# Optimization experiments

Measured on AMD Instinct MI355X. Metric: run time of the kernel, lower is better.

The kernel has to match this reference:

```python
import jax, jax.numpy as jnp
import numpy as np

B, L, D_MODEL, H = 2, 2048, 1024, 16
HD = D_MODEL // H  # head dim = 64


def setup_inputs() -> dict:
    key = jax.random.key(0)
    ks = jax.random.split(key, 11)
    s = 1.0 / np.sqrt(D_MODEL)
    inp = {
        "Q": jax.random.normal(ks[0], (B, L, D_MODEL), jnp.float32),
        "K": jax.random.normal(ks[1], (B, L, D_MODEL), jnp.float32),
        "V": jax.random.normal(ks[2], (B, L, D_MODEL), jnp.float32),
        "Wq": jax.random.normal(ks[3], (D_MODEL, D_MODEL), jnp.float32) * s,
        "bq": jnp.zeros((D_MODEL,), jnp.float32),
        "Wk": jax.random.normal(ks[4], (D_MODEL, D_MODEL), jnp.float32) * s,
        "bk": jnp.zeros((D_MODEL,), jnp.float32),
        "Wv": jax.random.normal(ks[5], (D_MODEL, D_MODEL), jnp.float32) * s,
        "bv": jnp.zeros((D_MODEL,), jnp.float32),
        "Wo": jax.random.normal(ks[6], (D_MODEL, D_MODEL), jnp.float32) * s,
        "bo": jnp.zeros((D_MODEL,), jnp.float32),
    }
    return inp


def _split_heads(x):
    # [B, L, H*D] -> [B, H, L, D]
    return x.reshape(B, L, H, HD).transpose(0, 2, 1, 3)


def reference(Q, K, V, Wq, bq, Wk, bk, Wv, bv, Wo, bo):
    q = _split_heads(Q @ Wq.T + bq)
    k = _split_heads(K @ Wk.T + bk)
    v = _split_heads(V @ Wv.T + bv)
    scale = 1.0 / jnp.sqrt(jnp.asarray(HD, q.dtype))
    # full [B, H, L, L] score matrix, as in the original bmm->softmax->bmm
    scores = jnp.einsum("bhqd,bhkd->bhqk", q, k) * scale
    attn = jax.nn.softmax(scores, axis=-1)
    o = jnp.einsum("bhqk,bhkd->bhqd", attn, v)
    o = o.transpose(0, 2, 1, 3).reshape(B, L, D_MODEL)  # concat heads
    return o @ Wo.T + bo
```

## Files before the change

### kernel.cpp

```cpp
#include <hip/hip_runtime.h>
#include <math.h>
#include <stdint.h>

typedef __bf16 bf16_t;
typedef __attribute__((ext_vector_type(2))) __bf16 bf16x2;
typedef __attribute__((ext_vector_type(8))) __bf16 bf16x8;
typedef __attribute__((ext_vector_type(4))) float f32x4;
typedef __attribute__((ext_vector_type(16))) float f32x16;
typedef __attribute__((address_space(1))) unsigned int gu32;
typedef __attribute__((address_space(3))) unsigned int lu32;

#define MFMA16(a, b, c) __builtin_amdgcn_mfma_f32_16x16x32_bf16((a), (b), (c), 0, 0, 0)
#define MFMA32(a, b, c) __builtin_amdgcn_mfma_f32_32x32x16_bf16((a), (b), (c), 0, 0, 0)

__device__ __forceinline__ void gll16(const void* g, void* l) {
    __builtin_amdgcn_global_load_lds((const gu32*)(uintptr_t)g,
                                     (lu32*)(uintptr_t)l, 16, 0, 0);
}

__device__ __forceinline__ bf16x8 ld_frag68(const bf16_t* p) {
    union { bf16x8 v; uint2 u[2]; } r;
    r.u[0] = *(const uint2*)p;
    r.u[1] = *(const uint2*)(p + 4);
    return r.v;
}

__global__ __launch_bounds__(256) void convert_all(
    const float* __restrict__ Q, const float* __restrict__ K, const float* __restrict__ V,
    const float* __restrict__ Wq, const float* __restrict__ Wk, const float* __restrict__ Wv,
    const float* __restrict__ Wo, bf16_t* __restrict__ dst) {
    size_t e0 = (size_t)blockIdx.x * 2048;
    const float* src; size_t off;
    if (e0 < 4194304)       { src = Q;  off = e0; }
    else if (e0 < 8388608)  { src = K;  off = e0 - 4194304; }
    else if (e0 < 12582912) { src = V;  off = e0 - 8388608; }
    else if (e0 < 13631488) { src = Wq; off = e0 - 12582912; }
    else if (e0 < 14680064) { src = Wk; off = e0 - 13631488; }
    else if (e0 < 15728640) { src = Wv; off = e0 - 14680064; }
    else                    { src = Wo; off = e0 - 15728640; }
#pragma unroll
    for (int p = 0; p < 2; ++p) {
        int t = p * 1024 + threadIdx.x * 4;
        float4 v = *(const float4*)(src + off + t);
        union { ushort4 u; bf16_t h[4]; } pk;
        pk.h[0] = (bf16_t)v.x; pk.h[1] = (bf16_t)v.y;
        pk.h[2] = (bf16_t)v.z; pk.h[3] = (bf16_t)v.w;
        *(ushort4*)(dst + e0 + t) = pk.u;
    }
}

__global__ __launch_bounds__(256) void qkv_gemm(
    const bf16_t* __restrict__ Qb, const bf16_t* __restrict__ Kb, const bf16_t* __restrict__ Vb,
    const bf16_t* __restrict__ Wqb, const bf16_t* __restrict__ Wkb, const bf16_t* __restrict__ Wvb,
    const float* __restrict__ bq, const float* __restrict__ bk, const float* __restrict__ bv,
    bf16_t* __restrict__ qo, bf16_t* __restrict__ ko, bf16_t* __restrict__ vT) {
    constexpr int Kdim = 1024, N = 1024;
    __shared__ __attribute__((aligned(16))) bf16_t smem[4 * 128 * 64];

    const int tid = threadIdx.x, wave = tid >> 6, lane = tid & 63;
    const int z = blockIdx.z;
    const bf16_t* A = (z == 0) ? Qb : (z == 1) ? Kb : Vb;
    const bf16_t* W = (z == 0) ? Wqb : (z == 1) ? Wkb : Wvb;
    const float* bias = (z == 0) ? bq : (z == 1) ? bk : bv;
    const int bm = blockIdx.x * 128, bn = blockIdx.y * 128;
    const int l16 = lane & 15, quad = lane >> 4;
    const int wm = (wave >> 1) * 64, wn = (wave & 1) * 64;
    const int grow = lane >> 3;
    const int gcol = (((lane & 7) ^ grow)) * 8;
    const int rsw = l16 & 7;

    f32x4 acc[4][4] = {};

    auto stage = [&](int k0, bf16_t* As, bf16_t* Bs) {
#pragma unroll
        for (int j = 0; j < 4; ++j) {
            int chunk = wave * 4 + j;
            int row = chunk * 8 + grow;
            gll16(A + (size_t)(bm + row) * Kdim + k0 + gcol, As + chunk * 512);
            gll16(W + (size_t)(bn + row) * Kdim + k0 + gcol, Bs + chunk * 512);
        }
    };
    auto compute = [&](const bf16_t* As, const bf16_t* Bs) {
#pragma unroll
        for (int ks = 0; ks < 64; ks += 32) {
            const int sl = ((ks >> 3) + quad);
            const int so = (sl ^ rsw) * 8;
            bf16x8 af[4], bf[4];
#pragma unroll
            for (int i = 0; i < 4; ++i)
                af[i] = *(const bf16x8*)&As[(wm + i * 16 + l16) * 64 + so];
#pragma unroll
            for (int i = 0; i < 4; ++i)
                bf[i] = *(const bf16x8*)&Bs[(wn + i * 16 + l16) * 64 + so];
#pragma unroll
            for (int i = 0; i < 4; ++i)
#pragma unroll
                for (int j = 0; j < 4; ++j)
                    acc[i][j] = MFMA16(af[i], bf[j], acc[i][j]);
        }
    };

    stage(0, smem, smem + 8192);
    asm volatile("s_waitcnt vmcnt(0)" ::: "memory");
    __builtin_amdgcn_s_barrier();
    int cur = 0;
    for (int t = 0; t < 15; ++t) {
        bf16_t* nb = smem + (cur ^ 1) * 16384;
        stage((t + 1) * 64, nb, nb + 8192);
        bf16_t* cb = smem + cur * 16384;
        compute(cb, cb + 8192);
        asm volatile("s_waitcnt vmcnt(0)" ::: "memory");
        __builtin_amdgcn_s_barrier();
        cur ^= 1;
    }
    {
        bf16_t* cb = smem + cur * 16384;
        compute(cb, cb + 8192);
    }

    if (z < 2) {
        bf16_t* outp = (z == 0) ? qo : ko;
        const float sc = (z == 0) ? 0.18033688011112042f : 1.0f;
        constexpr int RST = 132;
#pragma unroll
        for (int p = 0; p < 2; ++p) {
            __syncthreads();
            if ((wave >> 1) == p) {
#pragma unroll
                for (int mi = 0; mi < 4; ++mi)
#pragma unroll
                    for (int nj = 0; nj < 4; ++nj) {
                        int col = wn + nj * 16 + l16;
                        float bv_ = bias[bn + col];
#pragma unroll
                        for (int r = 0; r < 4; ++r) {
                            int rp = mi * 16 + quad * 4 + r;
                            smem[rp * RST + col] = (bf16_t)((acc[mi][nj][r] + bv_) * sc);
                        }
                    }
            }
            __syncthreads();
            int rp = tid >> 2;
            int cb2 = (tid & 3) * 32;
            int row = bm + p * 64 + rp;
#pragma unroll
            for (int j = 0; j < 4; ++j) {
                uint2 lo = *(const uint2*)&smem[rp * RST + cb2 + j * 8];
                uint2 hi = *(const uint2*)&smem[rp * RST + cb2 + j * 8 + 4];
                *(uint4*)&outp[(size_t)row * N + bn + cb2 + j * 8] =
                    make_uint4(lo.x, lo.y, hi.x, hi.y);
            }
        }
    } else {
#pragma unroll
        for (int mi = 0; mi < 4; ++mi)
#pragma unroll
            for (int nj = 0; nj < 4; ++nj) {
                int col = bn + wn + nj * 16 + l16;
                int h = col >> 6, d = col & 63;
                float bv_ = bias[col];
                int row0 = bm + wm + mi * 16 + quad * 4;
                int bb = row0 >> 11, l = row0 & 2047;
                int lb = (l & ~12) | ((l & 4) << 1) | ((l & 8) >> 1);
                union { ushort4 u; bf16_t h4[4]; } pk;
#pragma unroll
                for (int r = 0; r < 4; ++r) pk.h4[r] = (bf16_t)(acc[mi][nj][r] + bv_);
                *(ushort4*)&vT[(((size_t)bb * 16 + h) * 64 + d) * 2048 + lb] = pk.u;
            }
    }
}

__global__ __launch_bounds__(256) void out_gemm(const bf16_t* __restrict__ A,
                                                const bf16_t* __restrict__ W,
                                                const float* __restrict__ bias,
                                                float* __restrict__ out) {
    constexpr int Kdim = 1024, N = 1024;
    __shared__ __attribute__((aligned(16))) bf16_t smem[2 * 12288];
    const int tid = threadIdx.x, wave = tid >> 6, lane = tid & 63;
    const int bm = blockIdx.x * 64, bn = blockIdx.y * 128;
    const int l16 = lane & 15, quad = lane >> 4;
    const int wm = (wave >> 1) * 32, wn = (wave & 1) * 64;
    const int grow = lane >> 3;
    const int gcol = (((lane & 7) ^ grow)) * 8;
    const int rsw = l16 & 7;
    f32x4 acc[2][4] = {};

    auto stage = [&](int k0, bf16_t* As, bf16_t* Bs) {
#pragma unroll
        for (int j = 0; j < 2; ++j) {
            int chunk = wave * 2 + j;
            int row = chunk * 8 + grow;
            gll16(A + (size_t)(bm + row) * Kdim + k0 + gcol, As + chunk * 512);
        }
#pragma unroll
        for (int j = 0; j < 4; ++j) {
            int chunk = wave * 4 + j;
            int row = chunk * 8 + grow;
            gll16(W + (size_t)(bn + row) * Kdim + k0 + gcol, Bs + chunk * 512);
        }
    };
    auto compute = [&](const bf16_t* As, const bf16_t* Bs) {
#pragma unroll
        for (int ks = 0; ks < 64; ks += 32) {
            const int so0 = ((((ks >> 3) + quad)) ^ rsw) * 8;
            bf16x8 af[2], bf[4];
#pragma unroll
            for (int i = 0; i < 2; ++i)
                af[i] = *(const bf16x8*)&As[(wm + i * 16 + l16) * 64 + so0];
#pragma unroll
            for (int i = 0; i < 4; ++i)
                bf[i] = *(const bf16x8*)&Bs[(wn + i * 16 + l16) * 64 + so0];
#pragma unroll
            for (int i = 0; i < 2; ++i)
#pragma unroll
                for (int j = 0; j < 4; ++j)
                    acc[i][j] = MFMA16(af[i], bf[j], acc[i][j]);
        }
    };

    stage(0, smem, smem + 4096);
    asm volatile("s_waitcnt vmcnt(0)" ::: "memory");
    __builtin_amdgcn_s_barrier();
    int cur = 0;
    for (int t = 0; t < 15; ++t) {
        bf16_t* nb = smem + (cur ^ 1) * 12288;
        stage((t + 1) * 64, nb, nb + 4096);
        bf16_t* cb = smem + cur * 12288;
        compute(cb, cb + 4096);
        asm volatile("s_waitcnt vmcnt(0)" ::: "memory");
        __builtin_amdgcn_s_barrier();
        cur ^= 1;
    }
    {
        bf16_t* cb = smem + cur * 12288;
        compute(cb, cb + 4096);
    }

#pragma unroll
    for (int mi = 0; mi < 2; ++mi)
#pragma unroll
        for (int nj = 0; nj < 4; ++nj) {
            int col = bn + wn + nj * 16 + l16;
            float bv_ = bias[col];
#pragma unroll
            for (int r = 0; r < 4; ++r) {
                int row = bm + wm + mi * 16 + quad * 4 + r;
                out[(size_t)row * N + col] = acc[mi][nj][r] + bv_;
            }
        }
}

__global__ __launch_bounds__(256, 2) void attn8(const bf16_t* __restrict__ qo,
                                                const bf16_t* __restrict__ ko,
                                                const bf16_t* __restrict__ vT,
                                                bf16_t* __restrict__ Op,
                                                float* __restrict__ lpp) {
    constexpr int L = 2048, D = 1024, ST = 68;
    constexpr int BUF = 2 * 64 * ST;
    __shared__ __attribute__((aligned(16))) bf16_t smem[2 * BUF];

    const int tid = threadIdx.x, wave = tid >> 6, lane = tid & 63;
    const int l31 = lane & 31, hi = lane >> 5;
    const int b = blockIdx.x >> 4, h = blockIdx.x & 15;
    const int q0 = blockIdx.y * 256;
    const int split = blockIdx.z;
    bf16_t* Opart = Op + (size_t)split * 4194304;
    float* lpart = lpp + split * 65536;

    const int rloc = tid >> 2, cg = tid & 3;
    const bf16_t* kbase = ko + ((size_t)b * L + rloc) * D + h * 64 + cg * 16;
    const bf16_t* vbase = vT + (((size_t)b * 16 + h) * 64 + rloc) * L + cg * 16;

    bf16x8 qfa[4], qfb[4];
    {
        const bf16_t* qa = qo + ((size_t)b * L + q0 + wave * 32 + l31) * D + h * 64 + hi * 8;
        const bf16_t* qb2 = qa + (size_t)128 * D;
#pragma unroll
        for (int ks = 0; ks < 4; ++ks) {
            qfa[ks] = *(const bf16x8*)(qa + ks * 16);
            qfb[ks] = *(const bf16x8*)(qb2 + ks * 16);
        }
    }

    f32x16 o0a{}, o1a{}, o0b{}, o1b{};
    float lpla = 0.f, lplb = 0.f;

    const int kt0 = split * 16, kt1 = kt0 + 16;

    uint4 ka, kc, va, vc;
    auto gload = [&](int kt) {
        const size_t koff = (size_t)(kt * 64) * D;
        const int voff = kt * 64;
        ka = *(const uint4*)(kbase + koff);
        kc = *(const uint4*)(kbase + koff + 8);
        va = *(const uint4*)(vbase + voff);
        vc = *(const uint4*)(vbase + voff + 8);
    };
    auto swrite = [&](bf16_t* buf) {
        bf16_t* kd = &buf[rloc * ST + cg * 16];
        bf16_t* vd = &buf[64 * ST + rloc * ST + cg * 16];
        *(uint2*)(kd + 0)  = make_uint2(ka.x, ka.y);
        *(uint2*)(kd + 4)  = make_uint2(ka.z, ka.w);
        *(uint2*)(kd + 8)  = make_uint2(kc.x, kc.y);
        *(uint2*)(kd + 12) = make_uint2(kc.z, kc.w);
        *(uint2*)(vd + 0)  = make_uint2(va.x, va.y);
        *(uint2*)(vd + 4)  = make_uint2(va.z, va.w);
        *(uint2*)(vd + 8)  = make_uint2(vc.x, vc.y);
        *(uint2*)(vd + 12) = make_uint2(vc.z, vc.w);
    };

    gload(kt0);
    swrite(smem);
    gload(kt0 + 1 < kt1 ? kt0 + 1 : kt1 - 1);
    asm volatile("s_waitcnt lgkmcnt(0)" ::: "memory");
    __builtin_amdgcn_s_barrier();

    int cur = 0;
    for (int kt = kt0; kt < kt1; ++kt) {
        swrite(smem + (cur ^ 1) * BUF);
        gload(kt + 2 < kt1 ? kt + 2 : kt1 - 1);
        const bf16_t* ksm = smem + cur * BUF;
        const bf16_t* vsm = ksm + 64 * ST;

        f32x16 s0a{}, s1a{}, s0b{}, s1b{};
        __builtin_amdgcn_s_setprio(1);
#pragma unroll
        for (int ks = 0; ks < 4; ++ks) {
            bf16x8 k0 = ld_frag68(&ksm[l31 * ST + ks * 16 + hi * 8]);
            bf16x8 k1 = ld_frag68(&ksm[(32 + l31) * ST + ks * 16 + hi * 8]);
            s0a = MFMA32(k0, qfa[ks], s0a);
            s1a = MFMA32(k1, qfa[ks], s1a);
            s0b = MFMA32(k0, qfb[ks], s0b);
            s1b = MFMA32(k1, qfb[ks], s1b);
        }
        __builtin_amdgcn_s_setprio(0);

#pragma unroll
        for (int t = 0; t < 4; ++t) {
            union { bf16x8 v; bf16_t e[8]; } pfa, pfb;
#pragma unroll
            for (int j = 0; j < 8; ++j) {
                float sva = (t < 2) ? s0a[(t & 1) * 8 + j] : s1a[(t & 1) * 8 + j];
                float svb = (t < 2) ? s0b[(t & 1) * 8 + j] : s1b[(t & 1) * 8 + j];
                float pa = __builtin_amdgcn_exp2f(sva);
                float pb = __builtin_amdgcn_exp2f(svb);
                lpla += pa; lplb += pb;
                pfa.e[j] = (bf16_t)pa;
                pfb.e[j] = (bf16_t)pb;
            }
            bf16x8 v0 = ld_frag68(&vsm[l31 * ST + t * 16 + hi * 8]);
            bf16x8 v1 = ld_frag68(&vsm[(32 + l31) * ST + t * 16 + hi * 8]);
            __builtin_amdgcn_s_setprio(1);
            o0a = MFMA32(v0, pfa.v, o0a);
            o1a = MFMA32(v1, pfa.v, o1a);
            o0b = MFMA32(v0, pfb.v, o0b);
            o1b = MFMA32(v1, pfb.v, o1b);
            __builtin_amdgcn_s_setprio(0);
        }

        asm volatile("s_waitcnt lgkmcnt(0)" ::: "memory");
        __builtin_amdgcn_s_barrier();
        cur ^= 1;
    }

    lpla += __shfl_xor(lpla, 32, 64);
    lplb += __shfl_xor(lplb, 32, 64);
    if (hi == 0) {
        lpart[((size_t)b * 16 + h) * 2048 + q0 + wave * 32 + l31] = lpla;
        lpart[((size_t)b * 16 + h) * 2048 + q0 + 128 + wave * 32 + l31] = lplb;
    }

    __syncthreads();
    bf16_t* ew = smem + wave * (32 * ST);
#pragma unroll
    for (int r = 0; r < 16; r += 2) {
        int d = (r & 3) + 8 * (r >> 2) + 4 * hi;
        *(bf16x2*)&ew[l31 * ST + d] = bf16x2{(bf16_t)o0a[r], (bf16_t)o0a[r + 1]};
        *(bf16x2*)&ew[l31 * ST + 32 + d] = bf16x2{(bf16_t)o1a[r], (bf16_t)o1a[r + 1]};
    }
#pragma unroll
    for (int p = 0; p < 4; ++p) {
        int rr = p * 8 + (lane >> 3);
        int cc = (lane & 7) * 8;
        uint2 lo = *(const uint2*)&ew[rr * ST + cc];
        uint2 hi2 = *(const uint2*)&ew[rr * ST + cc + 4];
        *(uint4*)&Opart[((size_t)b * L + q0 + wave * 32 + rr) * D + h * 64 + cc] =
            make_uint4(lo.x, lo.y, hi2.x, hi2.y);
    }
#pragma unroll
    for (int r = 0; r < 16; r += 2) {
        int d = (r & 3) + 8 * (r >> 2) + 4 * hi;
        *(bf16x2*)&ew[l31 * ST + d] = bf16x2{(bf16_t)o0b[r], (bf16_t)o0b[r + 1]};
        *(bf16x2*)&ew[l31 * ST + 32 + d] = bf16x2{(bf16_t)o1b[r], (bf16_t)o1b[r + 1]};
    }
#pragma unroll
    for (int p = 0; p < 4; ++p) {
        int rr = p * 8 + (lane >> 3);
        int cc = (lane & 7) * 8;
        uint2 lo = *(const uint2*)&ew[rr * ST + cc];
        uint2 hi2 = *(const uint2*)&ew[rr * ST + cc + 4];
        *(uint4*)&Opart[((size_t)b * L + q0 + 128 + wave * 32 + rr) * D + h * 64 + cc] =
            make_uint4(lo.x, lo.y, hi2.x, hi2.y);
    }
}

__global__ __launch_bounds__(256) void combine(const bf16_t* __restrict__ Op,
                                               const float* __restrict__ lpp,
                                               bf16_t* __restrict__ Ob) {
    const size_t c = (size_t)blockIdx.x * 256 + threadIdx.x;
    const int bl = (int)(c >> 7);
    const int h = ((int)c >> 3) & 15;
    const int bb = bl >> 11, l = bl & 2047;
    const int li = (bb * 16 + h) * 2048 + l;
    const float inv = 1.f / (lpp[li] + lpp[65536 + li]);
    union { uint4 u; bf16_t h8[8]; } a, b, o;
    a.u = *(const uint4*)(Op + c * 8);
    b.u = *(const uint4*)(Op + 4194304 + c * 8);
#pragma unroll
    for (int i = 0; i < 8; ++i)
        o.h8[i] = (bf16_t)(((float)a.h8[i] + (float)b.h8[i]) * inv);
    *(uint4*)(Ob + c * 8) = o.u;
}

extern "C" void kernel_launch(void* const* d_in, const int* in_sizes, int n_in,
                              void* d_out, int out_size, void* d_ws, size_t ws_size,
                              hipStream_t stream) {
    const float* Q  = (const float*)d_in[0];
    const float* Kx = (const float*)d_in[1];
    const float* V  = (const float*)d_in[2];
    const float* Wq = (const float*)d_in[3];
    const float* bq = (const float*)d_in[4];
    const float* Wk = (const float*)d_in[5];
    const float* bk = (const float*)d_in[6];
    const float* Wv = (const float*)d_in[7];
    const float* bv = (const float*)d_in[8];
    const float* Wo = (const float*)d_in[9];
    const float* bo = (const float*)d_in[10];

    bf16_t* ws0 = (bf16_t*)d_ws;
    bf16_t* Qb  = ws0;
    bf16_t* Kb  = ws0 + 4194304;
    bf16_t* Vb  = ws0 + 8388608;
    bf16_t* Wqb = ws0 + 12582912;
    bf16_t* Wkb = ws0 + 13631488;
    bf16_t* Wvb = ws0 + 14680064;
    bf16_t* Wob = ws0 + 15728640;
    bf16_t* vT  = ws0 + 16777216;
    bf16_t* Op  = Qb;
    bf16_t* Obf = Vb;
    float*  lpp = (float*)Wqb;
    bf16_t* qo = (bf16_t*)d_out;
    bf16_t* ko = qo + 4194304;

    convert_all<<<8192, 256, 0, stream>>>(Q, Kx, V, Wq, Wk, Wv, Wo, ws0);
    qkv_gemm<<<dim3(32, 8, 3), 256, 0, stream>>>(Qb, Kb, Vb, Wqb, Wkb, Wvb,
                                                 bq, bk, bv, qo, ko, vT);
    attn8<<<dim3(32, 8, 2), 256, 0, stream>>>(qo, ko, vT, Op, lpp);
    combine<<<2048, 256, 0, stream>>>(Op, lpp, Obf);
    out_gemm<<<dim3(64, 8), 256, 0, stream>>>(Obf, Wob, bo, (float*)d_out);
}
```

Baseline: 217.6 us.

## Fuse split-KV combine into output GEMM and single-buffer QKV GEMM

Removes the separate combine kernel. The output projection GEMM now loads both partial attention outputs and the softmax denominators, normalises them in registers and writes the A tile to shared memory itself. This saves one launch and a full write and read of the combined bf16 activation. Separately, the QKV GEMM drops its double-buffered async-load pipeline for a single buffer with syncthreads around each stage, which halves its LDS use but exposes load latency.

```diff
diff --git a/kernel.cpp b/kernel.cpp
--- a/kernel.cpp
+++ b/kernel.cpp
@@ -55,7 +55,9 @@
     const float* __restrict__ bq, const float* __restrict__ bk, const float* __restrict__ bv,
     bf16_t* __restrict__ qo, bf16_t* __restrict__ ko, bf16_t* __restrict__ vT) {
     constexpr int Kdim = 1024, N = 1024;
-    __shared__ __attribute__((aligned(16))) bf16_t smem[4 * 128 * 64];
+    __shared__ __attribute__((aligned(16))) bf16_t smem[2 * 128 * 64];
+    bf16_t* As = smem;
+    bf16_t* Bs = smem + 8192;
 
     const int tid = threadIdx.x, wave = tid >> 6, lane = tid & 63;
     const int z = blockIdx.z;
@@ -71,7 +73,7 @@
 
     f32x4 acc[4][4] = {};
 
-    auto stage = [&](int k0, bf16_t* As, bf16_t* Bs) {
+    for (int k0 = 0; k0 < Kdim; k0 += 64) {
 #pragma unroll
         for (int j = 0; j < 4; ++j) {
             int chunk = wave * 4 + j;
@@ -79,12 +81,10 @@
             gll16(A + (size_t)(bm + row) * Kdim + k0 + gcol, As + chunk * 512);
             gll16(W + (size_t)(bn + row) * Kdim + k0 + gcol, Bs + chunk * 512);
         }
-    };
-    auto compute = [&](const bf16_t* As, const bf16_t* Bs) {
+        __syncthreads();
 #pragma unroll
         for (int ks = 0; ks < 64; ks += 32) {
-            const int sl = ((ks >> 3) + quad);
-            const int so = (sl ^ rsw) * 8;
+            const int so = (((ks >> 3) + quad) ^ rsw) * 8;
             bf16x8 af[4], bf[4];
 #pragma unroll
             for (int i = 0; i < 4; ++i)
@@ -98,24 +98,7 @@
                 for (int j = 0; j < 4; ++j)
                     acc[i][j] = MFMA16(af[i], bf[j], acc[i][j]);
         }
-    };
-
-    stage(0, smem, smem + 8192);
-    asm volatile("s_waitcnt vmcnt(0)" ::: "memory");
-    __builtin_amdgcn_s_barrier();
-    int cur = 0;
-    for (int t = 0; t < 15; ++t) {
-        bf16_t* nb = smem + (cur ^ 1) * 16384;
-        stage((t + 1) * 64, nb, nb + 8192);
-        bf16_t* cb = smem + cur * 16384;
-        compute(cb, cb + 8192);
-        asm volatile("s_waitcnt vmcnt(0)" ::: "memory");
-        __builtin_amdgcn_s_barrier();
-        cur ^= 1;
-    }
-    {
-        bf16_t* cb = smem + cur * 16384;
-        compute(cb, cb + 8192);
+        __syncthreads();
     }
 
     if (z < 2) {
@@ -170,7 +153,8 @@
     }
 }
 
-__global__ __launch_bounds__(256) void out_gemm(const bf16_t* __restrict__ A,
+__global__ __launch_bounds__(256) void out_gemm(const bf16_t* __restrict__ Op,
+                                                const float* __restrict__ lpp,
                                                 const bf16_t* __restrict__ W,
                                                 const float* __restrict__ bias,
                                                 float* __restrict__ out) {
@@ -185,13 +169,37 @@
     const int rsw = l16 & 7;
     f32x4 acc[2][4] = {};
 
-    auto stage = [&](int k0, bf16_t* As, bf16_t* Bs) {
-#pragma unroll
-        for (int j = 0; j < 2; ++j) {
-            int chunk = wave * 2 + j;
-            int row = chunk * 8 + grow;
-            gll16(A + (size_t)(bm + row) * Kdim + k0 + gcol, As + chunk * 512);
-        }
+    const int arow0 = bm + (wave * 2 + 0) * 8 + grow;
+    const int arow1 = bm + (wave * 2 + 1) * 8 + grow;
+
+    uint4 a0p, a0q, a1p, a1q;
+    float ivn0, ivn1;
+
+    auto loadA = [&](int k0) {
+        const int h = k0 >> 6;
+        a0p = *(const uint4*)(Op + (size_t)arow0 * Kdim + k0 + gcol);
+        a0q = *(const uint4*)(Op + 4194304 + (size_t)arow0 * Kdim + k0 + gcol);
+        a1p = *(const uint4*)(Op + (size_t)arow1 * Kdim + k0 + gcol);
+        a1q = *(const uint4*)(Op + 4194304 + (size_t)arow1 * Kdim + k0 + gcol);
+        const int li0 = ((arow0 >> 11) * 16 + h) * 2048 + (arow0 & 2047);
+        const int li1 = ((arow1 >> 11) * 16 + h) * 2048 + (arow1 & 2047);
+        ivn0 = 1.f / (lpp[li0] + lpp[65536 + li0]);
+        ivn1 = 1.f / (lpp[li1] + lpp[65536 + li1]);
+    };
+    auto writeA = [&](bf16_t* As) {
+        union { uint4 u; bf16_t h8[8]; } x, y, w0, w1;
+        x.u = a0p; y.u = a0q;
+#pragma unroll
+        for (int i = 0; i < 8; ++i)
+            w0.h8[i] = (bf16_t)(((float)x.h8[i] + (float)y.h8[i]) * ivn0);
+        x.u = a1p; y.u = a1q;
+#pragma unroll
+        for (int i = 0; i < 8; ++i)
+            w1.h8[i] = (bf16_t)(((float)x.h8[i] + (float)y.h8[i]) * ivn1);
+        *(uint4*)&As[(wave * 2 + 0) * 512 + lane * 8] = w0.u;
+        *(uint4*)&As[(wave * 2 + 1) * 512 + lane * 8] = w1.u;
+    };
+    auto stageW = [&](int k0, bf16_t* Bs) {
 #pragma unroll
         for (int j = 0; j < 4; ++j) {
             int chunk = wave * 4 + j;
@@ -202,7 +210,7 @@
     auto compute = [&](const bf16_t* As, const bf16_t* Bs) {
 #pragma unroll
         for (int ks = 0; ks < 64; ks += 32) {
-            const int so0 = ((((ks >> 3) + quad)) ^ rsw) * 8;
+            const int so0 = (((ks >> 3) + quad) ^ rsw) * 8;
             bf16x8 af[2], bf[4];
 #pragma unroll
             for (int i = 0; i < 2; ++i)
@@ -218,17 +226,20 @@
         }
     };
 
-    stage(0, smem, smem + 4096);
-    asm volatile("s_waitcnt vmcnt(0)" ::: "memory");
-    __builtin_amdgcn_s_barrier();
+    loadA(0);
+    stageW(0, smem + 4096);
+    writeA(smem);
+    __syncthreads();
     int cur = 0;
     for (int t = 0; t < 15; ++t) {
         bf16_t* nb = smem + (cur ^ 1) * 12288;
-        stage((t + 1) * 64, nb, nb + 4096);
+        loadA((t + 1) * 64);
+        stageW((t + 1) * 64, nb + 4096);
         bf16_t* cb = smem + cur * 12288;
         compute(cb, cb + 4096);
+        writeA(nb);
         asm volatile("s_waitcnt vmcnt(0)" ::: "memory");
-        __builtin_amdgcn_s_barrier();
+        __syncthreads();
         cur ^= 1;
     }
     {
@@ -404,24 +415,6 @@
     }
 }
 
-__global__ __launch_bounds__(256) void combine(const bf16_t* __restrict__ Op,
-                                               const float* __restrict__ lpp,
-                                               bf16_t* __restrict__ Ob) {
-    const size_t c = (size_t)blockIdx.x * 256 + threadIdx.x;
-    const int bl = (int)(c >> 7);
-    const int h = ((int)c >> 3) & 15;
-    const int bb = bl >> 11, l = bl & 2047;
-    const int li = (bb * 16 + h) * 2048 + l;
-    const float inv = 1.f / (lpp[li] + lpp[65536 + li]);
-    union { uint4 u; bf16_t h8[8]; } a, b, o;
-    a.u = *(const uint4*)(Op + c * 8);
-    b.u = *(const uint4*)(Op + 4194304 + c * 8);
-#pragma unroll
-    for (int i = 0; i < 8; ++i)
-        o.h8[i] = (bf16_t)(((float)a.h8[i] + (float)b.h8[i]) * inv);
-    *(uint4*)(Ob + c * 8) = o.u;
-}
-
 extern "C" void kernel_launch(void* const* d_in, const int* in_sizes, int n_in,
                               void* d_out, int out_size, void* d_ws, size_t ws_size,
                               hipStream_t stream) {
@@ -447,7 +440,6 @@
     bf16_t* Wob = ws0 + 15728640;
     bf16_t* vT  = ws0 + 16777216;
     bf16_t* Op  = Qb;
-    bf16_t* Obf = Vb;
     float*  lpp = (float*)Wqb;
     bf16_t* qo = (bf16_t*)d_out;
     bf16_t* ko = qo + 4194304;
@@ -456,6 +448,5 @@
     qkv_gemm<<<dim3(32, 8, 3), 256, 0, stream>>>(Qb, Kb, Vb, Wqb, Wkb, Wvb,
                                                  bq, bk, bv, qo, ko, vT);
     attn8<<<dim3(32, 8, 2), 256, 0, stream>>>(qo, ko, vT, Op, lpp);
-    combine<<<2048, 256, 0, stream>>>(Op, lpp, Obf);
-    out_gemm<<<dim3(64, 8), 256, 0, stream>>>(Obf, Wob, bo, (float*)d_out);
-}
+    out_gemm<<<dim3(64, 8), 256, 0, stream>>>(Op, lpp, Wob, bo, (float*)d_out);
+}
```

Measured after the change: 223.8 us. 2.8% more time.
